# Optimization experiments

Measured on AMD Instinct MI355X. Metric: run time of the kernel, lower is better.

Reference implementation:

```python
import jax, jax.numpy as jnp
import numpy as np

N = 50000          # nodes
E_RAND = 600000    # random edges (self-loops appended -> E = 650000)
H, C = 2, 128      # heads, per-head channels
IN, OUT = 128, 40
SLOPE = 0.2        # PyG GATv2 default negative_slope
EPS = 1e-16


def setup_inputs() -> dict:
    key = jax.random.key(0)
    ks = jax.random.split(key, 16)
    x = jax.random.normal(ks[0], (N, IN), jnp.float32)
    src = jax.random.randint(ks[1], (E_RAND,), 0, N)
    dst = jax.random.randint(ks[2], (E_RAND,), 0, N)
    loops = jnp.arange(N)
    edge_index = jnp.stack([jnp.concatenate([src, loops]),
                            jnp.concatenate([dst, loops])]).astype(jnp.int64)

    def glorot(k, shape):
        fan = shape[0] + shape[-1]
        return jax.random.normal(k, shape, jnp.float32) * jnp.sqrt(2.0 / fan)

    return {
        "x": x, "edge_index": edge_index,
        "Wl1": glorot(ks[3], (IN, H * C)), "Wr1": glorot(ks[4], (IN, H * C)),
        "att1": glorot(ks[5], (H, C)), "b1": jnp.zeros((H * C,), jnp.float32),
        "Wl2": glorot(ks[6], (H * C, H * C)), "Wr2": glorot(ks[7], (H * C, H * C)),
        "att2": glorot(ks[8], (H, C)), "b2": jnp.zeros((H * C,), jnp.float32),
        "W3": glorot(ks[9], (H * C, C)), "b3": jnp.zeros((C,), jnp.float32),
        "W4": glorot(ks[10], (C, OUT)), "b4": jnp.zeros((OUT,), jnp.float32),
    }


def gatv2_conv(x, src, dst, Wl, Wr, att, b):
    # x: [N, F]; lin_l -> source messages, lin_r -> target. Output concat heads.
    xl = (x @ Wl).reshape(-1, H, C)              # [N,H,C]
    xr = (x @ Wr).reshape(-1, H, C)
    e = jax.nn.leaky_relu(xl[src] + xr[dst], SLOPE)   # [E,H,C]
    score = jnp.einsum('ehc,hc->eh', e, att)          # [E,H]
    # segment softmax over incoming edges of each dst node
    m = jax.ops.segment_max(score, dst, num_segments=N)       # [N,H]
    a = jnp.exp(score - m[dst])
    denom = jax.ops.segment_sum(a, dst, num_segments=N)
    alpha = a / (denom[dst] + EPS)                              # [E,H]
    out = jax.ops.segment_sum(alpha[:, :, None] * xl[src], dst, num_segments=N)
    return out.reshape(-1, H * C) + b


def reference(x, edge_index, Wl1, Wr1, att1, b1, Wl2, Wr2, att2, b2, W3, b3, W4, b4):
    src, dst = edge_index[0], edge_index[1]
    h = jax.nn.relu(gatv2_conv(x, src, dst, Wl1, Wr1, att1, b1))   # dropout: eval mode
    h = jax.nn.relu(gatv2_conv(h, src, dst, Wl2, Wr2, att2, b2))
    h = h @ W3 + b3
    h = h @ W4 + b4
    return jax.nn.sigmoid(h)   # [N, OUT]
```

## Files before the change

kernel.cpp:

```cpp
#include <hip/hip_runtime.h>
#include <hip/hip_bf16.h>
#include <math.h>

typedef __attribute__((ext_vector_type(4))) float f32x4;
typedef __attribute__((ext_vector_type(8))) short s16x8;
typedef __attribute__((ext_vector_type(8))) unsigned short u16x8;

#define CAP 48

__device__ inline unsigned short f2b(float f) {
    union { float f; unsigned u; } x; x.f = f;
    unsigned r = x.u + 0x7FFF + ((x.u >> 16) & 1);
    return (unsigned short)(r >> 16);
}
__device__ inline float b2f(unsigned short b) {
    union { unsigned u; float f; } x; x.u = ((unsigned)b) << 16; return x.f;
}

__device__ inline void gload_lds16(const void* g, void* l) {
    __builtin_amdgcn_global_load_lds(
        (const __attribute__((address_space(1))) void*)g,
        (__attribute__((address_space(3))) void*)l, 16, 0, 0);
}

#define GBM 128
#define GBN 128
#define GBK 64

__global__ __launch_bounds__(256) void gemm_mfma(
    const unsigned short* __restrict__ A, const unsigned short* __restrict__ Bt,
    const float* __restrict__ bias, void* __restrict__ Cout, void* __restrict__ Cout2,
    int M, int Nn, int K, int split, int mode)
{
    __shared__ unsigned short As[GBM * GBK];
    __shared__ unsigned short Bs[GBN * GBK];
    const int tid = threadIdx.x;
    const int lane = tid & 63;
    const int w = tid >> 6, wm = w >> 1, wn = w & 1;
    const int row0 = blockIdx.y * GBM, col0 = blockIdx.x * GBN;
    const int l15 = lane & 15, l7 = lane & 7, lhi = lane >> 4;

    f32x4 acc[4][4] = {};

    for (int k0 = 0; k0 < K; k0 += GBK) {
        #pragma unroll
        for (int i = 0; i < 4; i++) {
            int L = i * 256 + tid;
            int row = L >> 3;
            int c = (L & 7) ^ (row & 7);
            int gr = row0 + row; gr = gr < M ? gr : M - 1;
            gload_lds16(A + (size_t)gr * K + k0 + c * 8, (char*)As + L * 16);
        }
        #pragma unroll
        for (int i = 0; i < 4; i++) {
            int L = i * 256 + tid;
            int row = L >> 3;
            int c = (L & 7) ^ (row & 7);
            gload_lds16(Bt + (size_t)(col0 + row) * K + k0 + c * 8, (char*)Bs + L * 16);
        }
        __syncthreads();
        #pragma unroll
        for (int kk = 0; kk < 2; kk++) {
            s16x8 af[4], bf[4];
            #pragma unroll
            for (int i = 0; i < 4; i++) {
                int slot = (wm * 64 + i * 16 + l15) * 8 + ((kk * 4 + lhi) ^ l7);
                af[i] = *(const s16x8*)((const char*)As + slot * 16);
            }
            #pragma unroll
            for (int j = 0; j < 4; j++) {
                int slot = (wn * 64 + j * 16 + l15) * 8 + ((kk * 4 + lhi) ^ l7);
                bf[j] = *(const s16x8*)((const char*)Bs + slot * 16);
            }
            #pragma unroll
            for (int i = 0; i < 4; i++)
                #pragma unroll
                for (int j = 0; j < 4; j++)
                    acc[i][j] = __builtin_amdgcn_mfma_f32_16x16x32_bf16(
                        af[i], bf[j], acc[i][j], 0, 0, 0);
        }
        __syncthreads();
    }

    if (mode == 0) {
        unsigned short* C  = (unsigned short*)Cout;
        unsigned short* C2 = (unsigned short*)Cout2;
        const int ld2 = Nn - split;
        #pragma unroll
        for (int i = 0; i < 4; i++)
            #pragma unroll
            for (int r = 0; r < 4; r++) {
                int row = row0 + wm * 64 + i * 16 + lhi * 4 + r;
                if (row >= M) continue;
                #pragma unroll
                for (int j = 0; j < 4; j++) {
                    int col = col0 + wn * 64 + j * 16 + l15;
                    unsigned short val = f2b(acc[i][j][r]);
                    if (col < split) C[(size_t)row * split + col] = val;
                    else             C2[(size_t)row * ld2 + (col - split)] = val;
                }
            }
    } else {
        float* C = (float*)Cout;
        #pragma unroll
        for (int i = 0; i < 4; i++)
            #pragma unroll
            for (int r = 0; r < 4; r++) {
                int row = row0 + wm * 64 + i * 16 + lhi * 4 + r;
                if (row >= M) continue;
                #pragma unroll
                for (int j = 0; j < 4; j++) {
                    int col = col0 + wn * 64 + j * 16 + l15;
                    if (col >= split) continue;
                    float v = acc[i][j][r] + bias[col];
                    C[(size_t)row * split + col] = 1.f / (1.f + __expf(-v));
                }
            }
    }
}

#define PA 6250
#define PB 6282
#define PC 6346
#define PD 6371
#define PE 6499

__global__ __launch_bounds__(256) void k_prep(
    const float* __restrict__ x,
    const float* __restrict__ Wl1, const float* __restrict__ Wr1,
    const float* __restrict__ Wl2, const float* __restrict__ Wr2,
    const float* __restrict__ W3,  const float* __restrict__ W4,
    const float* __restrict__ b3,  const float* __restrict__ b4,
    unsigned short* __restrict__ xbf,
    unsigned short* __restrict__ Wcat1, unsigned short* __restrict__ Wcat2,
    unsigned short* __restrict__ W34t, float* __restrict__ b34,
    int* __restrict__ cnt, int Nn)
{
    __shared__ float w4c[128];
    const int b = blockIdx.x, tid = threadIdx.x;

    if (b < PA) {
        int i = b * 1024 + tid * 4;
        float4 v = *(const float4*)&x[i];
        ushort4 o = { f2b(v.x), f2b(v.y), f2b(v.z), f2b(v.w) };
        *(ushort4*)&xbf[i] = o;
    } else if (b < PB) {
        int base = (b - PA) * 2048 + tid * 8;
        #pragma unroll
        for (int j = 0; j < 8; j++) {
            int e = base + j;
            int ep = e & 32767, n = ep >> 7, k = ep & 127;
            const float* srcp = (e < 32768) ? Wl1 : Wr1;
            Wcat1[e] = f2b(srcp[k * 256 + n]);
        }
    } else if (b < PC) {
        int base = (b - PB) * 2048 + tid * 8;
        #pragma unroll
        for (int j = 0; j < 8; j++) {
            int e = base + j;
            int ep = e & 65535, n = ep >> 8, k = ep & 255;
            const float* srcp = (e < 65536) ? Wl2 : Wr2;
            Wcat2[e] = f2b(srcp[k * 256 + n]);
        }
    } else if (b < PD) {
        int base = (b - PC) * 2048 + tid * 8;
        #pragma unroll
        for (int j = 0; j < 8; j++) {
            int i = base + j;
            if (i < Nn) cnt[i] = 0;
        }
    } else {
        int n = b - PD;
        if (tid < 128) w4c[tid] = (n < 40) ? W4[tid * 40 + n] : 0.f;
        __syncthreads();
        float s = 0.f;
        if (n < 40) {
            const float4* p = (const float4*)&W3[(size_t)tid * 128];
            #pragma unroll
            for (int j = 0; j < 32; j++) {
                float4 v = p[j];
                s = fmaf(v.x, w4c[j * 4 + 0], s);
                s = fmaf(v.y, w4c[j * 4 + 1], s);
                s = fmaf(v.z, w4c[j * 4 + 2], s);
                s = fmaf(v.w, w4c[j * 4 + 3], s);
            }
        }
        W34t[(size_t)n * 256 + tid] = f2b(s);
        if (tid == 0 && n < 40) {
            float t = b4[n];
            for (int j = 0; j < 128; j++) t = fmaf(b3[j], w4c[j], t);
            b34[n] = t;
        }
    }
}

__global__ void k_fillb(const int* __restrict__ src, const int* __restrict__ dstv, int E,
    int* __restrict__ cnt, int* __restrict__ colA)
{
    int e = blockIdx.x * blockDim.x + threadIdx.x;
    if (e >= E) return;
    int d = dstv[e];
    int slot = atomicAdd(&cnt[d], 1);
    colA[d * CAP + slot] = src[e];
}

__global__ __launch_bounds__(256) void k_attn(const unsigned short* __restrict__ xl,
    const unsigned short* __restrict__ xr, const float* __restrict__ att,
    const int* __restrict__ cnt, const int* __restrict__ colA,
    const float* __restrict__ bias, int Nn, unsigned short* __restrict__ outp)
{
    int n = blockIdx.x * 4 + (threadIdx.x >> 6);
    int lane = threadIdx.x & 63;
    if (n >= Nn) return;
    const int lh = lane & 31;
    const int h  = lane >> 5;
    int r0 = n * CAP;
    int r1 = r0 + cnt[n];

    const float LOG2E = 1.4426950408889634f;
    u16x8 xb = *(const u16x8*)&xr[(size_t)n * 256 + lh * 8];
    float xrv[8], w[8];
    #pragma unroll
    for (int k = 0; k < 8; k++) { xrv[k] = b2f(xb[k]); w[k] = att[lh * 8 + k] * LOG2E; }

    float m = -INFINITY, l = 0.f;
    float acc[8] = {};

    auto update = [&](const u16x8& vb) {
        float v[8];
        #pragma unroll
        for (int k = 0; k < 8; k++) v[k] = b2f(vb[k]);
        float dot = 0.f;
        #pragma unroll
        for (int k = 0; k < 8; k++) {
            float t = v[k] + xrv[k];
            t = fmaxf(t, 0.2f * t);
            dot = fmaf(t, w[k], dot);
        }
        #pragma unroll
        for (int off = 1; off <= 8; off <<= 1) dot += __shfl_xor(dot, off);
        if (__ballot(dot > m + 8.f)) {
            float mn = fmaxf(m, dot);
            float sc = exp2f(m - mn);
            float we = exp2f(dot - mn);
            l = l * sc + we;
            #pragma unroll
            for (int k = 0; k < 8; k++) acc[k] = acc[k] * sc + we * v[k];
            m = mn;
        } else {
            float we = exp2f(dot - m);
            l += we;
            #pragma unroll
            for (int k = 0; k < 8; k++) acc[k] = fmaf(we, v[k], acc[k]);
        }
    };

    int s = r0 + h;
    for (; s + 2 < r1; s += 4) {
        int c0 = colA[s], c1 = colA[s + 2];
        u16x8 v0 = *(const u16x8*)&xl[(size_t)c0 * 256 + lh * 8];
        u16x8 v1 = *(const u16x8*)&xl[(size_t)c1 * 256 + lh * 8];
        update(v0);
        update(v1);
    }
    for (; s < r1; s += 2) {
        int c = colA[s];
        u16x8 v = *(const u16x8*)&xl[(size_t)c * 256 + lh * 8];
        update(v);
    }

    float mq = (m == -INFINITY) ? -1e30f : m;
    float mo = __shfl_xor(mq, 32);
    float lo = __shfl_xor(l, 32);
    float ms = fmaxf(mq, mo);
    float es = exp2f(mq - ms), eo = exp2f(mo - ms);
    float lt = l * es + lo * eo + 1e-16f;
    float inv = 1.f / lt;

    u16x8 o;
    #pragma unroll
    for (int k = 0; k < 8; k++) {
        float other = __shfl_xor(acc[k], 32);
        float r = (acc[k] * es + other * eo) * inv + bias[lh * 8 + k];
        o[k] = f2b(fmaxf(r, 0.f));
    }
    if (h == 0) *(u16x8*)&outp[(size_t)n * 256 + lh * 8] = o;
}

extern "C" void kernel_launch(void* const* d_in, const int* in_sizes, int n_in,
                              void* d_out, int out_size, void* d_ws, size_t ws_size,
                              hipStream_t stream)
{
    const float* x    = (const float*)d_in[0];
    const int*   ei   = (const int*)d_in[1];
    const float* Wl1  = (const float*)d_in[2];
    const float* Wr1  = (const float*)d_in[3];
    const float* att1 = (const float*)d_in[4];
    const float* b1   = (const float*)d_in[5];
    const float* Wl2  = (const float*)d_in[6];
    const float* Wr2  = (const float*)d_in[7];
    const float* att2 = (const float*)d_in[8];
    const float* b2   = (const float*)d_in[9];
    const float* W3   = (const float*)d_in[10];
    const float* b3   = (const float*)d_in[11];
    const float* W4   = (const float*)d_in[12];
    const float* b4   = (const float*)d_in[13];

    const int N = in_sizes[0] / 128;
    const int E = in_sizes[1] / 2;
    const int* src  = ei;
    const int* dstv = ei + E;
    float* out = (float*)d_out;

    char* ws = (char*)d_ws;
    size_t o = 0;
    auto alloc = [&](size_t bytes) -> void* {
        void* p = ws + o;
        o += (bytes + 255) & ~(size_t)255;
        return p;
    };
    unsigned short* xbf    = (unsigned short*)alloc((size_t)N * 128 * 2);
    unsigned short* Wcat1  = (unsigned short*)alloc(512 * 128 * 2);
    unsigned short* Wcat2  = (unsigned short*)alloc(512 * 256 * 2);
    unsigned short* W34t   = (unsigned short*)alloc(128 * 256 * 2);
    float*          b34    = (float*)alloc(128 * 4);
    unsigned short* xlb    = (unsigned short*)alloc((size_t)N * 256 * 2);
    unsigned short* xrb    = (unsigned short*)alloc((size_t)N * 256 * 2);
    unsigned short* h1b    = (unsigned short*)alloc((size_t)N * 256 * 2);
    unsigned short* h2b    = (unsigned short*)alloc((size_t)N * 256 * 2);
    int* cnt    = (int*)alloc((size_t)N * 4);
    int* colA   = (int*)alloc((size_t)N * CAP * 4);

    dim3 blk(256);

    k_prep<<<PE, blk, 0, stream>>>(x, Wl1, Wr1, Wl2, Wr2, W3, W4, b3, b4,
                                   xbf, Wcat1, Wcat2, W34t, b34, cnt, N);

    k_fillb<<<(E + 255) / 256, blk, 0, stream>>>(src, dstv, E, cnt, colA);

    const int gy = (N + GBM - 1) / GBM;

    gemm_mfma<<<dim3(4, gy), blk, 0, stream>>>(xbf, Wcat1, nullptr, xlb, xrb,
                                               N, 512, 128, 256, 0);
    k_attn<<<(N + 3) / 4, blk, 0, stream>>>(xlb, xrb, att1, cnt, colA, b1, N, h1b);

    gemm_mfma<<<dim3(4, gy), blk, 0, stream>>>(h1b, Wcat2, nullptr, xlb, xrb,
                                               N, 512, 256, 256, 0);
    k_attn<<<(N + 3) / 4, blk, 0, stream>>>(xlb, xrb, att2, cnt, colA, b2, N, h2b);

    gemm_mfma<<<dim3(1, gy), blk, 0, stream>>>(h2b, W34t, b34, out, nullptr,
                                               N, 128, 256, 40, 2);
}
```

Before: 283.4 us.

## Widen GEMM tile to 256 columns with 512 threads, pre-shift gather indices

```diff
diff --git a/kernel.cpp b/kernel.cpp
--- a/kernel.cpp
+++ b/kernel.cpp
@@ -24,10 +24,10 @@
 }
 
 #define GBM 128
-#define GBN 128
+#define GBN 256
 #define GBK 64
 
-__global__ __launch_bounds__(256) void gemm_mfma(
+__global__ __launch_bounds__(512) void gemm_mfma(
     const unsigned short* __restrict__ A, const unsigned short* __restrict__ Bt,
     const float* __restrict__ bias, void* __restrict__ Cout, void* __restrict__ Cout2,
     int M, int Nn, int K, int split, int mode)
@@ -36,7 +36,7 @@
     __shared__ unsigned short Bs[GBN * GBK];
     const int tid = threadIdx.x;
     const int lane = tid & 63;
-    const int w = tid >> 6, wm = w >> 1, wn = w & 1;
+    const int w = tid >> 6, wm = w >> 2, wn = w & 3;
     const int row0 = blockIdx.y * GBM, col0 = blockIdx.x * GBN;
     const int l15 = lane & 15, l7 = lane & 7, lhi = lane >> 4;
 
@@ -44,8 +44,8 @@
 
     for (int k0 = 0; k0 < K; k0 += GBK) {
         #pragma unroll
-        for (int i = 0; i < 4; i++) {
-            int L = i * 256 + tid;
+        for (int i = 0; i < 2; i++) {
+            int L = i * 512 + tid;
             int row = L >> 3;
             int c = (L & 7) ^ (row & 7);
             int gr = row0 + row; gr = gr < M ? gr : M - 1;
@@ -53,7 +53,7 @@
         }
         #pragma unroll
         for (int i = 0; i < 4; i++) {
-            int L = i * 256 + tid;
+            int L = i * 512 + tid;
             int row = L >> 3;
             int c = (L & 7) ^ (row & 7);
             gload_lds16(Bt + (size_t)(col0 + row) * K + k0 + c * 8, (char*)Bs + L * 16);
@@ -122,8 +122,7 @@
 #define PA 6250
 #define PB 6282
 #define PC 6346
-#define PD 6371
-#define PE 6499
+#define PE 6602
 
 __global__ __launch_bounds__(256) void k_prep(
     const float* __restrict__ x,
@@ -133,8 +132,7 @@
     const float* __restrict__ b3,  const float* __restrict__ b4,
     unsigned short* __restrict__ xbf,
     unsigned short* __restrict__ Wcat1, unsigned short* __restrict__ Wcat2,
-    unsigned short* __restrict__ W34t, float* __restrict__ b34,
-    int* __restrict__ cnt, int Nn)
+    unsigned short* __restrict__ W34t, float* __restrict__ b34)
 {
     __shared__ float w4c[128];
     const int b = blockIdx.x, tid = threadIdx.x;
@@ -162,19 +160,12 @@
             const float* srcp = (e < 65536) ? Wl2 : Wr2;
             Wcat2[e] = f2b(srcp[k * 256 + n]);
         }
-    } else if (b < PD) {
-        int base = (b - PC) * 2048 + tid * 8;
-        #pragma unroll
-        for (int j = 0; j < 8; j++) {
-            int i = base + j;
-            if (i < Nn) cnt[i] = 0;
-        }
     } else {
-        int n = b - PD;
-        if (tid < 128) w4c[tid] = (n < 40) ? W4[tid * 40 + n] : 0.f;
-        __syncthreads();
-        float s = 0.f;
+        int n = b - PC;
         if (n < 40) {
+            if (tid < 128) w4c[tid] = W4[tid * 40 + n];
+            __syncthreads();
+            float s = 0.f;
             const float4* p = (const float4*)&W3[(size_t)tid * 128];
             #pragma unroll
             for (int j = 0; j < 32; j++) {
@@ -184,12 +175,14 @@
                 s = fmaf(v.z, w4c[j * 4 + 2], s);
                 s = fmaf(v.w, w4c[j * 4 + 3], s);
             }
-        }
-        W34t[(size_t)n * 256 + tid] = f2b(s);
-        if (tid == 0 && n < 40) {
-            float t = b4[n];
-            for (int j = 0; j < 128; j++) t = fmaf(b3[j], w4c[j], t);
-            b34[n] = t;
+            W34t[(size_t)n * 256 + tid] = f2b(s);
+            if (tid == 0) {
+                float t = b4[n];
+                for (int j = 0; j < 128; j++) t = fmaf(b3[j], w4c[j], t);
+                b34[n] = t;
+            }
+        } else {
+            W34t[(size_t)n * 256 + tid] = 0;
         }
     }
 }
@@ -201,7 +194,7 @@
     if (e >= E) return;
     int d = dstv[e];
     int slot = atomicAdd(&cnt[d], 1);
-    colA[d * CAP + slot] = src[e];
+    colA[d * CAP + slot] = src[e] << 8;
 }
 
 __global__ __launch_bounds__(256) void k_attn(const unsigned short* __restrict__ xl,
@@ -258,14 +251,14 @@
     int s = r0 + h;
     for (; s + 2 < r1; s += 4) {
         int c0 = colA[s], c1 = colA[s + 2];
-        u16x8 v0 = *(const u16x8*)&xl[(size_t)c0 * 256 + lh * 8];
-        u16x8 v1 = *(const u16x8*)&xl[(size_t)c1 * 256 + lh * 8];
+        u16x8 v0 = *(const u16x8*)&xl[(size_t)c0 + lh * 8];
+        u16x8 v1 = *(const u16x8*)&xl[(size_t)c1 + lh * 8];
         update(v0);
         update(v1);
     }
     for (; s < r1; s += 2) {
         int c = colA[s];
-        u16x8 v = *(const u16x8*)&xl[(size_t)c * 256 + lh * 8];
+        u16x8 v = *(const u16x8*)&xl[(size_t)c + lh * 8];
         update(v);
     }
 
@@ -322,7 +315,7 @@
     unsigned short* xbf    = (unsigned short*)alloc((size_t)N * 128 * 2);
     unsigned short* Wcat1  = (unsigned short*)alloc(512 * 128 * 2);
     unsigned short* Wcat2  = (unsigned short*)alloc(512 * 256 * 2);
-    unsigned short* W34t   = (unsigned short*)alloc(128 * 256 * 2);
+    unsigned short* W34t   = (unsigned short*)alloc(256 * 256 * 2);
     float*          b34    = (float*)alloc(128 * 4);
     unsigned short* xlb    = (unsigned short*)alloc((size_t)N * 256 * 2);
     unsigned short* xrb    = (unsigned short*)alloc((size_t)N * 256 * 2);
@@ -333,21 +326,22 @@
 
     dim3 blk(256);
 
+    hipMemsetAsync(cnt, 0, (size_t)N * 4, stream);
     k_prep<<<PE, blk, 0, stream>>>(x, Wl1, Wr1, Wl2, Wr2, W3, W4, b3, b4,
-                                   xbf, Wcat1, Wcat2, W34t, b34, cnt, N);
+                                   xbf, Wcat1, Wcat2, W34t, b34);
 
     k_fillb<<<(E + 255) / 256, blk, 0, stream>>>(src, dstv, E, cnt, colA);
 
     const int gy = (N + GBM - 1) / GBM;
 
-    gemm_mfma<<<dim3(4, gy), blk, 0, stream>>>(xbf, Wcat1, nullptr, xlb, xrb,
-                                               N, 512, 128, 256, 0);
+    gemm_mfma<<<dim3(2, gy), dim3(512), 0, stream>>>(xbf, Wcat1, nullptr, xlb, xrb,
+                                                     N, 512, 128, 256, 0);
     k_attn<<<(N + 3) / 4, blk, 0, stream>>>(xlb, xrb, att1, cnt, colA, b1, N, h1b);
 
-    gemm_mfma<<<dim3(4, gy), blk, 0, stream>>>(h1b, Wcat2, nullptr, xlb, xrb,
-                                               N, 512, 256, 256, 0);
+    gemm_mfma<<<dim3(2, gy), dim3(512), 0, stream>>>(h1b, Wcat2, nullptr, xlb, xrb,
+                                                     N, 512, 256, 256, 0);
     k_attn<<<(N + 3) / 4, blk, 0, stream>>>(xlb, xrb, att2, cnt, colA, b2, N, h2b);
 
-    gemm_mfma<<<dim3(1, gy), blk, 0, stream>>>(h2b, W34t, b34, out, nullptr,
-                                               N, 128, 256, 40, 2);
-}
+    gemm_mfma<<<dim3(1, gy), dim3(512), 0, stream>>>(h2b, W34t, b34, out, nullptr,
+                                                     N, 128, 256, 40, 2);
+}
```

Result: faster. 273.7 us (-3.4%).
